# Kernel optimization log

Measured on AMD Instinct MI355X. Metric: run time of the kernel, lower is better.

The kernel has to match this reference:

```python
import jax, jax.numpy as jnp
import numpy as np

N = 20000; E = 160000; C = 64; SH = 9; NB = 8
S_DIM = 16; MS_HID = 64; FC_HID = 64
RATE = 0.1; LAMBDA = 0.5; R_MAX = 5.0; EV_PER = 16
K = int(RATE * N)          # static master-node count (top-k selection)
E_V = EV_PER * K           # static virtual-edge budget


def _safe_len(vec):
    # smooth norm, safe under autodiff at zero-length edges (self loops)
    return jnp.sqrt(jnp.sum(vec * vec, axis=-1, keepdims=True) + 1e-12)


def _sh(vec):
    # real spherical harmonics lmax=2, 'component' normalization, on unit vectors
    n = vec / _safe_len(vec)
    x, y, z = n[:, 0], n[:, 1], n[:, 2]
    s3 = jnp.sqrt(3.0); s15 = jnp.sqrt(15.0); s5 = jnp.sqrt(5.0)
    return jnp.stack([
        jnp.ones_like(x),
        s3 * x, s3 * y, s3 * z,
        s15 * x * y, s15 * y * z, 0.5 * s5 * (3 * z * z - 1.0),
        s15 * x * z, 0.5 * s15 * (x * x - y * y),
    ], axis=-1)  # [E, 9]


def _bessel(r):
    # Bessel radial basis with p=6 polynomial cutoff envelope; r: [E,1]
    n = jnp.arange(1, NB + 1, dtype=r.dtype)
    b = jnp.sqrt(2.0 / R_MAX) * jnp.sin(n * jnp.pi * r / R_MAX) / jnp.clip(r, 1e-9)
    u = jnp.clip(r / R_MAX, 0.0, 1.0); p = 6.0
    env = 1.0 - (p + 1) * (p + 2) / 2 * u ** p + p * (p + 2) * u ** (p + 1) - p * (p + 1) / 2 * u ** (p + 2)
    return b * env  # [E, NB]


def _conv(h, src, dst, sh, ef, emask, n_nodes, fc_w1, fc_b1, fc_w2, fc_b2, lin_w):
    # TFN-style tensor-product conv: per-edge weights from radial MLP,
    # message = flatten(h[dst] outer sh) * w -> linear -> scatter-mean to src
    w = jax.nn.relu(ef @ fc_w1 + fc_b1) @ fc_w2 + fc_b2            # [E, C*SH]
    tp = (h[dst][:, :, None] * sh[:, None, :]).reshape(sh.shape[0], -1) * w
    msg = (tp @ lin_w) * emask[:, None]                            # [E, C]
    agg = jax.ops.segment_sum(msg, src, num_segments=n_nodes)
    deg = jax.ops.segment_sum(emask, src, num_segments=n_nodes)
    return agg / jnp.clip(deg, 1.0)[:, None]


def setup_inputs() -> dict:
    key = jax.random.key(0)
    ks = jax.random.split(key, 12)
    def lin(k, i, o):
        return (jax.random.normal(k, (i, o), jnp.float32) / np.sqrt(i)).astype(jnp.float32)
    return {
        "h": jax.random.normal(ks[0], (N, C), jnp.float32),
        "pos": jax.random.uniform(ks[1], (N, 3), jnp.float32) * 10.0,
        "edge_index": jax.random.randint(ks[2], (2, E), 0, N, dtype=jnp.int32),
        "fc_w1": lin(ks[3], NB, FC_HID), "fc_b1": jnp.zeros((FC_HID,), jnp.float32),
        "fc_w2": lin(ks[4], FC_HID, C * SH), "fc_b2": jnp.zeros((C * SH,), jnp.float32),
        "lin_w": lin(ks[5], C * SH, C),
        "ms_w1": lin(ks[6], S_DIM, MS_HID), "ms_b1": jnp.zeros((MS_HID,), jnp.float32),
        "ms_w2": lin(ks[7], MS_HID, 1), "ms_b2": jnp.zeros((1,), jnp.float32),
        "vg_wq": lin(ks[8], S_DIM, S_DIM), "vg_wk": lin(ks[9], S_DIM, S_DIM),
    }


def reference(h, pos, fc_w1, fc_b1, fc_w2, fc_b2, lin_w,
              ms_w1, ms_b1, ms_w2, ms_b2, vg_wq, vg_wk, edge_index):
    src, dst = edge_index[0], edge_index[1]
    vec = pos[src] - pos[dst]
    sh = _sh(vec)
    ef = _bessel(_safe_len(vec))
    ones_e = jnp.ones((E,), h.dtype)
    h_update = _conv(h, src, dst, sh, ef, ones_e, N, fc_w1, fc_b1, fc_w2, fc_b2, lin_w)
    h_local = h_update + h  # in_dim == out_dim -> pad is a no-op

    # --- master selection (top-k by learned score; static K) ---
    h_sc = h_local[:, :S_DIM]
    score = jax.nn.sigmoid(
        (jax.nn.relu(h_sc @ ms_w1 + ms_b1) @ ms_w2 + ms_b2).squeeze(-1))  # [N]
    _, top_idx = jax.lax.top_k(score, K)
    node_mask = jnp.zeros((N,), h.dtype).at[top_idx].set(1.0)
    m = score * node_mask
    master_idx = jnp.sort(top_idx)

    # relabel full-graph ids -> master-subgraph ids (masked subgraph extraction)
    node2m = jnp.full((N,), -1, jnp.int32).at[master_idx].set(jnp.arange(K, dtype=jnp.int32))
    src_m, dst_m = node2m[src], node2m[dst]
    e_mask = ((src_m >= 0) & (dst_m >= 0)).astype(h.dtype)
    src_mc = jnp.where(src_m >= 0, src_m, 0)
    dst_mc = jnp.where(dst_m >= 0, dst_m, 0)
    adj = jnp.zeros((K, K), h.dtype).at[src_mc, dst_mc].add(e_mask)

    h_master = h_local[master_idx]
    pos_master = pos[master_idx]
    h_ms = h_master[:, :S_DIM]

    # --- virtual edge generation (attention, thresholded by lambda) ---
    q = h_ms @ vg_wq; kk = h_ms @ vg_wk
    attn = jax.nn.sigmoid(q @ kk.T / np.sqrt(S_DIM))  # [K, K]
    exist = (adj > 0) | jnp.eye(K, dtype=bool)
    A_virtual = jnp.where((~exist) & (attn > LAMBDA), 1.0, 0.0).astype(h.dtype)
    vvals, vidx = jax.lax.top_k((attn * A_virtual).reshape(-1), E_V)
    v_src = (vidx // K).astype(jnp.int32); v_dst = (vidx % K).astype(jnp.int32)
    v_mask = (vvals > 0).astype(h.dtype)

    src_all = jnp.concatenate([src_mc, v_src])
    dst_all = jnp.concatenate([dst_mc, v_dst])
    mask_all = jnp.concatenate([e_mask, v_mask])
    vec_m = pos_master[src_all] - pos_master[dst_all]
    sh_m = _sh(vec_m)
    ef_m = _bessel(_safe_len(vec_m))
    h_m_update = _conv(h_master, src_all, dst_all, sh_m, ef_m, mask_all, K,
                       fc_w1, fc_b1, fc_w2, fc_b2, lin_w)
    h_hier = h_m_update + h_master

    h_hier_exp = jnp.zeros_like(h_local).at[master_idx].set(h_hier)
    m_e = m[:, None]
    h_final = (1.0 - m_e) * h_local + m_e * h_hier_exp
    return (h_final, pos, A_virtual, m)
```

## Files before the change

kernel.cpp:

```cpp
#include <hip/hip_runtime.h>
#include <stdint.h>

constexpr int N_   = 20000;
constexpr int E_   = 160000;
constexpr int C_   = 64;
constexpr int K_   = 2000;
constexpr int EV_  = 32000;
constexpr int EALL_ = E_ + EV_;
constexpr int CSH_ = 576;
constexpr int TB_  = 48;

constexpr size_t OFF_AGG    = 0;
constexpr size_t OFF_DEG    = 5120000;
constexpr size_t OFF_AGGM   = 5200000;
constexpr size_t OFF_DEGM   = 5712000;
constexpr size_t OFF_RANK   = 5720000;
constexpr size_t OFF_MASKA  = 5800000;
constexpr size_t OFF_EXIST  = 6568000;
constexpr size_t OFF_HIST   = 10568000;
constexpr size_t OFF_STATE  = 10572096;
constexpr size_t ZERO_BYTES = 10572352;
constexpr size_t OFF_HLOCAL = 10572352;
constexpr size_t OFF_KEY    = 15692352;
constexpr size_t OFF_SCORE  = 15852352;
constexpr size_t OFF_N2M    = 15932352;
constexpr size_t OFF_MIDX   = 16012352;
constexpr size_t OFF_HM     = 16020352;
constexpr size_t OFF_POSM   = 16532352;
constexpr size_t OFF_Q      = 16556352;
constexpr size_t OFF_KBUF   = 16684352;
constexpr size_t OFF_SRCA   = 16812352;
constexpr size_t OFF_DSTA   = 17580352;
constexpr size_t OFF_TMAX   = 18348352;
constexpr size_t OFF_CAND   = 18410880;

struct RState {
    unsigned long long prefix;
    int R;
    unsigned int cand_count;
    unsigned int sel_count;
    int bin_thresh;
    unsigned int total;
    unsigned int pad;
};

__global__ void k_w0(const float* __restrict__ fc_b1, const float* __restrict__ fc_w2,
                     const float* __restrict__ fc_b2, int* __restrict__ w0nz)
{
    __shared__ float hid0[64];
    __shared__ int nz;
    int tid = threadIdx.x;
    if (tid == 0) nz = 0;
    if (tid < 64) hid0[tid] = fmaxf(fc_b1[tid], 0.0f);
    __syncthreads();
    if (tid < CSH_) {
        float acc = fc_b2[tid];
        for (int k = 0; k < 64; k++) acc += hid0[k] * fc_w2[k * CSH_ + tid];
        if (acc != 0.0f) atomicOr(&nz, 1);
    }
    __syncthreads();
    if (tid == 0) *w0nz = nz;
}

__global__ __launch_bounds__(256) void k_prep(
    int n_edges, const int* __restrict__ src, const int* __restrict__ dst,
    const float* __restrict__ mask, const float* __restrict__ posn,
    const int* __restrict__ w0nz, float* __restrict__ deg,
    float* __restrict__ edata, unsigned int* __restrict__ cnt)
{
    int e = blockIdx.x * 256 + threadIdx.x;
    bool valid = e < n_edges;
    int s_i = 0, d_i = 0; float msk = 0.0f;
    if (valid) {
        msk = mask ? mask[e] : 1.0f;
        if (msk != 0.0f) { s_i = src[e]; d_i = dst[e]; }
    }
    bool active = valid && (msk != 0.0f);

    float vx = 0.f, vy = 0.f, vz = 0.f;
    if (active) {
        vx = posn[s_i*3+0] - posn[d_i*3+0];
        vy = posn[s_i*3+1] - posn[d_i*3+1];
        vz = posn[s_i*3+2] - posn[d_i*3+2];
    }
    float r = sqrtf(vx*vx + vy*vy + vz*vz + 1e-12f);
    float invr = 1.0f / r;
    float x = vx*invr, y = vy*invr, z = vz*invr;
    const float s3 = 1.7320508075688772f, s15 = 3.872983346207417f, s5 = 2.23606797749979f;
    float sh[9];
    sh[0] = 1.0f; sh[1] = s3*x; sh[2] = s3*y; sh[3] = s3*z;
    sh[4] = s15*x*y; sh[5] = s15*y*z; sh[6] = 0.5f*s5*(3.0f*z*z - 1.0f);
    sh[7] = s15*x*z; sh[8] = 0.5f*s15*(x*x - y*y);

    float u = r * 0.2f; u = u > 1.0f ? 1.0f : u;
    float u2 = u*u, u6 = u2*u2*u2, u7 = u6*u, u8 = u7*u;
    float env = 1.0f - 28.0f*u6 + 48.0f*u7 - 21.0f*u8;
    float rc = r > 1e-9f ? r : 1e-9f;
    const float bpref = 0.6324555320336759f;
    const float PIov5 = 0.6283185307179586f;
    float ef[8];
    #pragma unroll
    for (int n = 0; n < 8; n++)
        ef[n] = bpref * sinf(PIov5 * r * (float)(n + 1)) / rc * env;

    if (active) atomicAdd(&deg[s_i], msk);

    bool contrib = active && !((env == 0.0f) && (*w0nz == 0));
    int lane = threadIdx.x & 63;
    unsigned long long b = __ballot(contrib);
    int wc = __popcll(b);
    int base = 0;
    if (lane == 0 && wc) base = (int)atomicAdd(cnt, (unsigned)wc);
    base = __shfl(base, 0);
    if (contrib) {
        int slot = base + __popcll(b & ((1ull << lane) - 1ull));
        float* p = edata + (size_t)slot * 20;
        #pragma unroll
        for (int n = 0; n < 8; n++) p[n] = ef[n];
        #pragma unroll
        for (int t = 0; t < 9; t++) p[8+t] = sh[t];
        p[17] = __int_as_float(s_i);
        p[18] = __int_as_float(d_i);
        p[19] = msk;
    }
}

__global__ __launch_bounds__(256, 2) void k_convg(
    const unsigned int* __restrict__ cnt, const float* __restrict__ edata,
    const float* __restrict__ hn,
    const float* __restrict__ fc_w1, const float* __restrict__ fc_b1,
    const float* __restrict__ fc_w2, const float* __restrict__ fc_b2,
    const float* __restrict__ lin_w, float* __restrict__ agg)
{
    __shared__ float s_misc[TB_ * 12];
    __shared__ float s_hid[TB_ * 68];
    __shared__ float s_hd[TB_ * 64];
    __shared__ float s_tp[TB_ * 68];
    __shared__ __align__(16) float s_w[4096];

    const int tid = threadIdx.x;
    const int oq = (tid & 15) * 4;
    const int eg = tid >> 4;

    const int nheavy = (int)*cnt;
    const int nblk = (nheavy + TB_ - 1) / TB_;

    for (int blk = blockIdx.x; blk < nblk; blk += gridDim.x) {
        const int ebase = blk * TB_;
        int nE = nheavy - ebase; if (nE > TB_) nE = TB_;

        for (int idx = tid; idx < TB_ * 12; idx += 256) {
            int e = idx / 12, f = idx - 12 * e;
            float v = 0.0f;
            if (e < nE) {
                const float* p = edata + (size_t)(ebase + e) * 20;
                v = (f < 9) ? p[8 + f] : (f == 9) ? p[17] : (f == 10) ? p[19] : 0.0f;
            }
            s_misc[idx] = v;
        }
        for (int idx = tid; idx < TB_ * 64; idx += 256) {
            int e = idx >> 6, k = idx & 63;
            float hv = 0.0f, hdv = 0.0f;
            if (e < nE) {
                const float* p = edata + (size_t)(ebase + e) * 20;
                float acc = fc_b1[k];
                #pragma unroll
                for (int n = 0; n < 8; n++) acc += p[n] * fc_w1[n * 64 + k];
                hv = fmaxf(acc, 0.0f);
                int dsti = __float_as_int(p[18]);
                hdv = hn[dsti * 64 + k];
            }
            s_hid[e * 68 + k] = hv;
            s_hd[e * 64 + k] = hdv;
        }
        float acc0[4] = {0,0,0,0}, acc1[4] = {0,0,0,0}, acc2[4] = {0,0,0,0};
        __syncthreads();

        for (int cj = 0; cj < 9; cj++) {
            const int j0 = cj * 64;
            for (int i4 = tid; i4 < 1024; i4 += 256) {
                int k = i4 >> 4, q4 = (i4 & 15) * 4;
                *reinterpret_cast<float4*>(&s_w[k * 64 + q4]) =
                    *reinterpret_cast<const float4*>(&fc_w2[k * CSH_ + j0 + q4]);
            }
            __syncthreads();

            float a0[4], a1[4], a2[4];
            #pragma unroll
            for (int p = 0; p < 4; p++) { float b = fc_b2[j0 + oq + p]; a0[p]=b; a1[p]=b; a2[p]=b; }
            #pragma unroll 4
            for (int k = 0; k < 64; k++) {
                float4 w4 = *reinterpret_cast<const float4*>(&s_w[k * 64 + oq]);
                float h0 = s_hid[eg * 68 + k];
                float h1 = s_hid[(eg + 16) * 68 + k];
                float h2 = s_hid[(eg + 32) * 68 + k];
                a0[0]+=h0*w4.x; a0[1]+=h0*w4.y; a0[2]+=h0*w4.z; a0[3]+=h0*w4.w;
                a1[0]+=h1*w4.x; a1[1]+=h1*w4.y; a1[2]+=h1*w4.z; a1[3]+=h1*w4.w;
                a2[0]+=h2*w4.x; a2[1]+=h2*w4.y; a2[2]+=h2*w4.z; a2[3]+=h2*w4.w;
            }
            #pragma unroll
            for (int p = 0; p < 4; p++) {
                int j = j0 + oq + p; int c = j / 9; int si = j - 9 * c;
                s_tp[eg * 68 + oq + p]        = s_hd[eg * 64 + c]        * s_misc[eg * 12 + si]        * a0[p];
                s_tp[(eg + 16) * 68 + oq + p] = s_hd[(eg + 16) * 64 + c] * s_misc[(eg + 16) * 12 + si] * a1[p];
                s_tp[(eg + 32) * 68 + oq + p] = s_hd[(eg + 32) * 64 + c] * s_misc[(eg + 32) * 12 + si] * a2[p];
            }
            __syncthreads();

            for (int i4 = tid; i4 < 1024; i4 += 256) {
                *reinterpret_cast<float4*>(&s_w[i4 * 4]) =
                    *reinterpret_cast<const float4*>(&lin_w[j0 * 64 + i4 * 4]);
            }
            __syncthreads();

            #pragma unroll 4
            for (int jj = 0; jj < 64; jj++) {
                float4 l4 = *reinterpret_cast<const float4*>(&s_w[jj * 64 + oq]);
                float t0 = s_tp[eg * 68 + jj];
                float t1 = s_tp[(eg + 16) * 68 + jj];
                float t2 = s_tp[(eg + 32) * 68 + jj];
                acc0[0]+=t0*l4.x; acc0[1]+=t0*l4.y; acc0[2]+=t0*l4.z; acc0[3]+=t0*l4.w;
                acc1[0]+=t1*l4.x; acc1[1]+=t1*l4.y; acc1[2]+=t1*l4.z; acc1[3]+=t1*l4.w;
                acc2[0]+=t2*l4.x; acc2[1]+=t2*l4.y; acc2[2]+=t2*l4.z; acc2[3]+=t2*l4.w;
            }
            __syncthreads();
        }

        {
            float mk = s_misc[eg * 12 + 10];
            if (mk != 0.0f) {
                int s = __float_as_int(s_misc[eg * 12 + 9]);
                #pragma unroll
                for (int p = 0; p < 4; p++) atomicAdd(&agg[s * 64 + oq + p], acc0[p] * mk);
            }
            mk = s_misc[(eg + 16) * 12 + 10];
            if (mk != 0.0f) {
                int s = __float_as_int(s_misc[(eg + 16) * 12 + 9]);
                #pragma unroll
                for (int p = 0; p < 4; p++) atomicAdd(&agg[s * 64 + oq + p], acc1[p] * mk);
            }
            mk = s_misc[(eg + 32) * 12 + 10];
            if (mk != 0.0f) {
                int s = __float_as_int(s_misc[(eg + 32) * 12 + 9]);
                #pragma unroll
                for (int p = 0; p < 4; p++) atomicAdd(&agg[s * 64 + oq + p], acc2[p] * mk);
            }
        }
        __syncthreads();
    }
}

__global__ __launch_bounds__(256) void k_hlscore(const float* __restrict__ h,
    const float* __restrict__ agg, const float* __restrict__ deg,
    const float* __restrict__ ms_w1, const float* __restrict__ ms_b1,
    const float* __restrict__ ms_w2, const float* __restrict__ ms_b2,
    float* __restrict__ h_local, float* __restrict__ score, unsigned long long* __restrict__ key)
{
    int wid = threadIdx.x >> 6, lane = threadIdx.x & 63;
    int n = blockIdx.x * 4 + wid;
    if (n >= N_) return;
    float d = fmaxf(deg[n], 1.0f);
    float hl = h[n*64 + lane] + agg[n*64 + lane] / d;
    h_local[n*64 + lane] = hl;
    float acc = ms_b1[lane];
    #pragma unroll
    for (int i = 0; i < 16; i++) acc += __shfl(hl, i) * ms_w1[i*64 + lane];
    acc = fmaxf(acc, 0.0f);
    float part = acc * ms_w2[lane];
    #pragma unroll
    for (int off = 32; off > 0; off >>= 1) part += __shfl_xor(part, off);
    if (lane == 0) {
        float s = part + ms_b2[0];
        float sc = 1.0f / (1.0f + expf(-s));
        score[n] = sc;
        key[n] = ((unsigned long long)__float_as_uint(sc) << 32)
               | (unsigned long long)(0xFFFFFFFFu - (unsigned)n);
    }
}

__global__ void k_rank(const unsigned long long* __restrict__ key, int* __restrict__ rankcnt)
{
    __shared__ unsigned long long tile[256];
    int i = blockIdx.x * 256 + threadIdx.x;
    int seg = blockIdx.y;
    int lo = seg * 1250, hi = lo + 1250;
    unsigned long long my = (i < N_) ? key[i] : ~0ull;
    int cnt = 0;
    for (int t0 = lo; t0 < hi; t0 += 256) {
        int idx = t0 + threadIdx.x;
        tile[threadIdx.x] = (idx < hi) ? key[idx] : 0ull;
        __syncthreads();
        int lim = hi - t0; if (lim > 256) lim = 256;
        for (int j = 0; j < lim; j++) cnt += (tile[j] > my) ? 1 : 0;
        __syncthreads();
    }
    if (i < N_ && cnt) atomicAdd(&rankcnt[i], cnt);
}

__global__ __launch_bounds__(1024) void k_scanfin(const int* __restrict__ rankcnt,
    const float* __restrict__ score, int* __restrict__ node2m, int* __restrict__ midx,
    float* __restrict__ m_out)
{
    __shared__ int ssum[1024];
    int tid = threadIdx.x;
    int start = tid * 20;
    int c = 0;
    for (int k = 0; k < 20; k++) {
        int idx = start + k;
        if (idx < N_) {
            int sel = (rankcnt[idx] < K_) ? 1 : 0;
            c += sel;
            m_out[idx] = sel ? score[idx] : 0.0f;
        }
    }
    ssum[tid] = c;
    __syncthreads();
    for (int off = 1; off < 1024; off <<= 1) {
        int v = (tid >= off) ? ssum[tid - off] : 0;
        __syncthreads();
        ssum[tid] += v;
        __syncthreads();
    }
    int run = ssum[tid] - c;
    for (int k = 0; k < 20; k++) {
        int idx = start + k;
        if (idx < N_) {
            if (rankcnt[idx] < K_) { node2m[idx] = run; midx[run] = idx; run++; }
            else node2m[idx] = -1;
        }
    }
}

__global__ __launch_bounds__(256) void k_mastex(const int* __restrict__ midx,
    const float* __restrict__ h_local, const float* __restrict__ pos,
    const float* __restrict__ vg_wq, const float* __restrict__ vg_wk,
    const int* __restrict__ src, const int* __restrict__ dst, const int* __restrict__ node2m,
    float* __restrict__ h_m, float* __restrict__ pos_m,
    float* __restrict__ qbuf, float* __restrict__ kbuf,
    int* __restrict__ src_all, int* __restrict__ dst_all,
    float* __restrict__ mask_all, unsigned char* __restrict__ exist)
{
    int b = blockIdx.x;
    if (b < 500) {
        int mi = b * 4 + (threadIdx.x >> 6);
        int lane = threadIdx.x & 63;
        int node = midx[mi];
        h_m[mi*64 + lane] = h_local[node*64 + lane];
        if (lane < 3) pos_m[mi*3 + lane] = pos[node*3 + lane];
        if (lane < 32) {
            int j = lane & 15;
            const float* wm = (lane < 16) ? vg_wq : vg_wk;
            float acc = 0.0f;
            #pragma unroll
            for (int i = 0; i < 16; i++) acc += h_local[node*64 + i] * wm[i*16 + j];
            if (lane < 16) qbuf[mi*16 + j] = acc; else kbuf[mi*16 + j] = acc;
        }
    } else {
        int e = (b - 500) * 256 + threadIdx.x;
        int sm = node2m[src[e]], dm = node2m[dst[e]];
        bool em = (sm >= 0) && (dm >= 0);
        int smc = sm >= 0 ? sm : 0;
        int dmc = dm >= 0 ? dm : 0;
        src_all[e] = smc; dst_all[e] = dmc; mask_all[e] = em ? 1.0f : 0.0f;
        if (em) exist[smc * K_ + dmc] = 1;
    }
}

constexpr int NTILE_ = (K_ / 16) * (K_ / 16);
__global__ __launch_bounds__(256) void k_attn1(const float* __restrict__ qbuf,
    const float* __restrict__ kbuf, const unsigned char* __restrict__ exist,
    float* __restrict__ Av, float* __restrict__ tmax, unsigned int* __restrict__ hist)
{
    constexpr int TBK = K_ / 16;
    __shared__ float sq[16][17], sk[16][17];
    __shared__ unsigned int lh[1024];
    __shared__ float wmax[4];
    int tid = threadIdx.x;
    for (int b = tid; b < 1024; b += 256) lh[b] = 0;

    for (int t = blockIdx.x; t < NTILE_; t += gridDim.x) {
        int bi = t / TBK, bj = t % TBK;
        int i0 = bi * 16, j0 = bj * 16;
        int r = tid >> 4, c = tid & 15;
        __syncthreads();
        sq[r][c] = qbuf[(i0 + r) * 16 + c];
        sk[r][c] = kbuf[(j0 + r) * 16 + c];
        __syncthreads();
        int ti = tid >> 4, tj = tid & 15;
        float dot = 0.0f;
        #pragma unroll
        for (int cc = 0; cc < 16; cc++) dot += sq[ti][cc] * sk[tj][cc];
        float attn = 1.0f / (1.0f + expf(-dot * 0.25f));
        int gi = i0 + ti, gj = j0 + tj;
        int flat = gi * K_ + gj;
        bool ex = (exist[flat] != 0) || (gi == gj);
        bool av = (!ex) && (attn > 0.5f);
        Av[flat] = av ? 1.0f : 0.0f;
        float cv = av ? attn : 0.0f;
        if (av) {
            unsigned bin = (__float_as_uint(attn) - 0x3F000000u) >> 13;
            if (bin > 1023u) bin = 1023u;
            atomicAdd(&lh[bin], 1u);
        }
        float wm = cv;
        #pragma unroll
        for (int off = 32; off > 0; off >>= 1) wm = fmaxf(wm, __shfl_xor(wm, off));
        int wid = tid >> 6, lane = tid & 63;
        if (lane == 0) wmax[wid] = wm;
        __syncthreads();
        if (tid == 0) tmax[t] = fmaxf(fmaxf(wmax[0], wmax[1]), fmaxf(wmax[2], wmax[3]));
    }
    __syncthreads();
    for (int b = tid; b < 1024; b += 256) {
        unsigned v = lh[b];
        if (v) atomicAdd(&hist[b], v);
    }
}

__global__ __launch_bounds__(1024) void k_bsel(const unsigned int* __restrict__ hist, RState* st)
{
    __shared__ unsigned int h[1024];
    int tid = threadIdx.x;
    h[tid] = hist[tid];
    __syncthreads();
    for (int off = 1; off < 1024; off <<= 1) {
        unsigned v = (tid + off < 1024) ? h[tid + off] : 0u;
        __syncthreads();
        h[tid] += v;
        __syncthreads();
    }
    unsigned total = h[0];
    int R = (total < (unsigned)EV_) ? (int)total : EV_;
    if (tid == 0) {
        st->R = R;
        st->total = total;
        st->cand_count = 0;
        st->sel_count = 0;
        if (R == 0) st->bin_thresh = 1024;
    }
    __syncthreads();
    if (R > 0) {
        unsigned hi = (tid == 1023) ? 0u : h[tid + 1];
        if ((int)h[tid] >= R && (int)hi < R) st->bin_thresh = tid;
    }
}

__global__ __launch_bounds__(256) void k_attn2(const float* __restrict__ qbuf,
    const float* __restrict__ kbuf, const unsigned char* __restrict__ exist,
    const float* __restrict__ tmax, RState* st, unsigned long long* __restrict__ cand)
{
    constexpr int TBK = K_ / 16;
    __shared__ float sq[16][17], sk[16][17];
    __shared__ int wb[4];
    __shared__ int bb;
    int tid = threadIdx.x;
    unsigned tbits = 0x3F000000u + ((unsigned)st->bin_thresh << 13);

    for (int t = blockIdx.x; t < NTILE_; t += gridDim.x) {
        if (__float_as_uint(tmax[t]) < tbits) continue;
        int bi = t / TBK, bj = t % TBK;
        int i0 = bi * 16, j0 = bj * 16;
        int r = tid >> 4, c = tid & 15;
        __syncthreads();
        sq[r][c] = qbuf[(i0 + r) * 16 + c];
        sk[r][c] = kbuf[(j0 + r) * 16 + c];
        __syncthreads();
        int ti = tid >> 4, tj = tid & 15;
        float dot = 0.0f;
        #pragma unroll
        for (int cc = 0; cc < 16; cc++) dot += sq[ti][cc] * sk[tj][cc];
        float attn = 1.0f / (1.0f + expf(-dot * 0.25f));
        int gi = i0 + ti, gj = j0 + tj;
        int flat = gi * K_ + gj;
        bool ex = (exist[flat] != 0) || (gi == gj);
        bool store = (!ex) && (attn > 0.5f) && (__float_as_uint(attn) >= tbits);

        unsigned long long keyv = ((unsigned long long)__float_as_uint(attn) << 32)
                                | (unsigned long long)(0xFFFFFFFFu - (unsigned)flat);
        int wid = tid >> 6, lane = tid & 63;
        unsigned long long b = __ballot(store);
        int wc = __popcll(b);
        if (lane == 0) wb[wid] = wc;
        __syncthreads();
        if (tid == 0) {
            int s = 0;
            for (int w = 0; w < 4; w++) { int cc2 = wb[w]; wb[w] = s; s += cc2; }
            bb = s ? (int)atomicAdd(&st->cand_count, (unsigned)s) : 0;
        }
        __syncthreads();
        if (store) {
            int slot = bb + wb[wid] + __popcll(b & ((1ull << lane) - 1ull));
            cand[slot] = keyv;
        }
    }
}

__global__ __launch_bounds__(1024) void k_radixsel(RState* st,
    const unsigned long long* __restrict__ cand,
    int* __restrict__ src_all, int* __restrict__ dst_all, float* __restrict__ mask_all)
{
    __shared__ unsigned int lh[256];
    __shared__ unsigned int suf[256];
    __shared__ unsigned long long s_pref;
    __shared__ int s_R;
    int tid = threadIdx.x;
    int n = (int)st->cand_count;
    int R = st->R;
    if (tid == 0) { s_pref = 0ull; s_R = R; }
    __syncthreads();

    if (R > 0) {
        for (int p = 0; p < 8; p++) {
            if (tid < 256) lh[tid] = 0;
            __syncthreads();
            unsigned long long pref = s_pref;
            int sh_d = 56 - 8 * p;
            for (int i = tid; i < n; i += 1024) {
                unsigned long long kv = cand[i];
                bool ok = (p == 0) || ((kv >> (sh_d + 8)) == (pref >> (sh_d + 8)));
                if (ok) atomicAdd(&lh[(unsigned)((kv >> sh_d) & 255ull)], 1u);
            }
            __syncthreads();
            if (tid < 256) suf[tid] = lh[tid];
            __syncthreads();
            for (int off = 1; off < 256; off <<= 1) {
                unsigned v = 0;
                if (tid < 256 && tid + off < 256) v = suf[tid + off];
                __syncthreads();
                if (tid < 256) suf[tid] += v;
                __syncthreads();
            }
            if (tid < 256) {
                int Rc = s_R;
                unsigned hi = (tid == 255) ? 0u : suf[tid + 1];
                if ((int)suf[tid] >= Rc && (int)hi < Rc) {
                    s_pref = pref | ((unsigned long long)(unsigned)tid << sh_d);
                    s_R = Rc - (int)hi;
                }
            }
            __syncthreads();
        }
    } else {
        if (tid == 0) s_pref = ~0ull;
        __syncthreads();
    }

    unsigned long long T = s_pref;
    int lane = tid & 63;
    for (int i0 = 0; i0 < n; i0 += 1024) {
        int i = i0 + tid;
        bool sel = (i < n) && (cand[i] >= T);
        unsigned long long b = __ballot(sel);
        int wc = __popcll(b);
        int basep = 0;
        if (lane == 0 && wc) basep = (int)atomicAdd(&st->sel_count, (unsigned)wc);
        basep = __shfl(basep, 0);
        if (sel) {
            int slot = basep + __popcll(b & ((1ull << lane) - 1ull));
            if (slot < EV_) {
                unsigned flat = 0xFFFFFFFFu - (unsigned)(cand[i] & 0xFFFFFFFFull);
                src_all[E_ + slot] = (int)(flat / (unsigned)K_);
                dst_all[E_ + slot] = (int)(flat % (unsigned)K_);
                mask_all[E_ + slot] = 1.0f;
            }
        }
    }
}

__global__ void k_finalpos(const float* __restrict__ h_local, const int* __restrict__ node2m,
    const float* __restrict__ aggm, const float* __restrict__ degm, const float* __restrict__ h_m,
    const float* __restrict__ m_out, const float* __restrict__ pos,
    float* __restrict__ out_h, float* __restrict__ out_pos)
{
    int idx = blockIdx.x * 256 + threadIdx.x;
    if (idx < N_ * 3) out_pos[idx] = pos[idx];
    if (idx >= N_ * C_) return;
    int i = idx >> 6, c = idx & 63;
    float mval = m_out[i];
    int mi = node2m[i];
    float hh = 0.0f;
    if (mi >= 0) hh = aggm[mi*64 + c] / fmaxf(degm[mi], 1.0f) + h_m[mi*64 + c];
    out_h[idx] = (1.0f - mval) * h_local[idx] + mval * hh;
}

extern "C" void kernel_launch(void* const* d_in, const int* in_sizes, int n_in,
                              void* d_out, int out_size, void* d_ws, size_t ws_size,
                              hipStream_t stream)
{
    (void)in_sizes; (void)n_in; (void)out_size; (void)ws_size;
    const float* h     = (const float*)d_in[0];
    const float* pos   = (const float*)d_in[1];
    const int*   eidx  = (const int*)d_in[2];
    const float* fc_w1 = (const float*)d_in[3];
    const float* fc_b1 = (const float*)d_in[4];
    const float* fc_w2 = (const float*)d_in[5];
    const float* fc_b2 = (const float*)d_in[6];
    const float* lin_w = (const float*)d_in[7];
    const float* ms_w1 = (const float*)d_in[8];
    const float* ms_b1 = (const float*)d_in[9];
    const float* ms_w2 = (const float*)d_in[10];
    const float* ms_b2 = (const float*)d_in[11];
    const float* vg_wq = (const float*)d_in[12];
    const float* vg_wk = (const float*)d_in[13];

    char* ws = (char*)d_ws;
    float* agg     = (float*)(ws + OFF_AGG);
    float* deg     = (float*)(ws + OFF_DEG);
    float* aggm    = (float*)(ws + OFF_AGGM);
    float* degm    = (float*)(ws + OFF_DEGM);
    int*   rankcnt = (int*)(ws + OFF_RANK);
    float* mask_all = (float*)(ws + OFF_MASKA);
    unsigned char* exist = (unsigned char*)(ws + OFF_EXIST);
    unsigned int* hist = (unsigned int*)(ws + OFF_HIST);
    RState* st     = (RState*)(ws + OFF_STATE);
    unsigned int* cnt0 = (unsigned int*)(ws + OFF_STATE + 64);
    unsigned int* cnt1 = (unsigned int*)(ws + OFF_STATE + 68);
    int*   w0nz    = (int*)(ws + OFF_STATE + 72);
    float* h_local = (float*)(ws + OFF_HLOCAL);
    unsigned long long* key = (unsigned long long*)(ws + OFF_KEY);
    float* score   = (float*)(ws + OFF_SCORE);
    int*   node2m  = (int*)(ws + OFF_N2M);
    int*   midx    = (int*)(ws + OFF_MIDX);
    float* h_m     = (float*)(ws + OFF_HM);
    float* pos_m   = (float*)(ws + OFF_POSM);
    float* qbuf    = (float*)(ws + OFF_Q);
    float* kbuf    = (float*)(ws + OFF_KBUF);
    int*   src_all = (int*)(ws + OFF_SRCA);
    int*   dst_all = (int*)(ws + OFF_DSTA);
    float* tmax    = (float*)(ws + OFF_TMAX);
    unsigned long long* cand = (unsigned long long*)(ws + OFF_CAND);
    float* edata   = (float*)(ws + OFF_CAND);

    float* out_h   = (float*)d_out;
    float* out_pos = out_h + (size_t)N_ * C_;
    float* out_av  = out_pos + (size_t)N_ * 3;
    float* out_m   = out_av + (size_t)K_ * K_;

    hipMemsetAsync(ws, 0, ZERO_BYTES, stream);

    k_w0<<<1, 576, 0, stream>>>(fc_b1, fc_w2, fc_b2, w0nz);

    k_prep<<<E_ / 256, 256, 0, stream>>>(E_, eidx, eidx + E_, nullptr, pos, w0nz, deg, edata, cnt0);
    k_convg<<<1024, 256, 0, stream>>>(cnt0, edata, h, fc_w1, fc_b1, fc_w2, fc_b2, lin_w, agg);

    k_hlscore<<<(N_ + 3) / 4, 256, 0, stream>>>(h, agg, deg, ms_w1, ms_b1, ms_w2, ms_b2,
                                                h_local, score, key);

    k_rank<<<dim3((N_ + 255) / 256, 16), 256, 0, stream>>>(key, rankcnt);
    k_scanfin<<<1, 1024, 0, stream>>>(rankcnt, score, node2m, midx, out_m);

    k_mastex<<<500 + E_ / 256, 256, 0, stream>>>(midx, h_local, pos, vg_wq, vg_wk,
        eidx, eidx + E_, node2m, h_m, pos_m, qbuf, kbuf, src_all, dst_all, mask_all, exist);

    k_attn1<<<1024, 256, 0, stream>>>(qbuf, kbuf, exist, out_av, tmax, hist);
    k_bsel<<<1, 1024, 0, stream>>>(hist, st);
    k_attn2<<<1024, 256, 0, stream>>>(qbuf, kbuf, exist, tmax, st, cand);
    k_radixsel<<<1, 1024, 0, stream>>>(st, cand, src_all, dst_all, mask_all);

    k_prep<<<EALL_ / 256, 256, 0, stream>>>(EALL_, src_all, dst_all, mask_all, pos_m, w0nz,
                                            degm, edata, cnt1);
    k_convg<<<1024, 256, 0, stream>>>(cnt1, edata, h_m, fc_w1, fc_b1, fc_w2, fc_b2, lin_w, aggm);

    k_finalpos<<<(N_ * C_ + 255) / 256, 256, 0, stream>>>(h_local, node2m, aggm, degm, h_m,
                                                          out_m, pos, out_h, out_pos);
}
```

Before: 764.0 us.

## Keep conv hidden and tensor-product tiles in registers via shuffles; simplify rank and scan

Result: slower. 826.5 us (+8.2%).

```diff
diff --git a/kernel.cpp b/kernel.cpp
--- a/kernel.cpp
+++ b/kernel.cpp
@@ -125,7 +125,7 @@
     }
 }
 
-__global__ __launch_bounds__(256, 2) void k_convg(
+__global__ __launch_bounds__(256, 3) void k_convg(
     const unsigned int* __restrict__ cnt, const float* __restrict__ edata,
     const float* __restrict__ hn,
     const float* __restrict__ fc_w1, const float* __restrict__ fc_b1,
@@ -133,14 +133,14 @@
     const float* __restrict__ lin_w, float* __restrict__ agg)
 {
     __shared__ float s_misc[TB_ * 12];
-    __shared__ float s_hid[TB_ * 68];
-    __shared__ float s_hd[TB_ * 64];
-    __shared__ float s_tp[TB_ * 68];
-    __shared__ __align__(16) float s_w[4096];
+    __shared__ float s_hd[TB_ * 66];
+    __shared__ __align__(16) float s_w2[4096];
+    __shared__ __align__(16) float s_lw[4096];
 
     const int tid = threadIdx.x;
     const int oq = (tid & 15) * 4;
     const int eg = tid >> 4;
+    const int r  = (tid & 63) >> 4;
 
     const int nheavy = (int)*cnt;
     const int nblk = (nheavy + TB_ - 1) / TB_;
@@ -149,6 +149,7 @@
         const int ebase = blk * TB_;
         int nE = nheavy - ebase; if (nE > TB_) nE = TB_;
 
+        __syncthreads();
         for (int idx = tid; idx < TB_ * 12; idx += 256) {
             int e = idx / 12, f = idx - 12 * e;
             float v = 0.0f;
@@ -160,70 +161,89 @@
         }
         for (int idx = tid; idx < TB_ * 64; idx += 256) {
             int e = idx >> 6, k = idx & 63;
-            float hv = 0.0f, hdv = 0.0f;
+            float hdv = 0.0f;
             if (e < nE) {
                 const float* p = edata + (size_t)(ebase + e) * 20;
-                float acc = fc_b1[k];
-                #pragma unroll
-                for (int n = 0; n < 8; n++) acc += p[n] * fc_w1[n * 64 + k];
-                hv = fmaxf(acc, 0.0f);
                 int dsti = __float_as_int(p[18]);
                 hdv = hn[dsti * 64 + k];
             }
-            s_hid[e * 68 + k] = hv;
-            s_hd[e * 64 + k] = hdv;
+            s_hd[e * 66 + k] = hdv;
+        }
+        float hid0[4], hid1[4], hid2[4];
+        {
+            const int es[3] = { eg, eg + 16, eg + 32 };
+            float* regs[3] = { hid0, hid1, hid2 };
+            #pragma unroll
+            for (int t = 0; t < 3; t++) {
+                int e = es[t];
+                if (e < nE) {
+                    const float* p = edata + (size_t)(ebase + e) * 20;
+                    float ef[8];
+                    #pragma unroll
+                    for (int n = 0; n < 8; n++) ef[n] = p[n];
+                    #pragma unroll
+                    for (int q = 0; q < 4; q++) {
+                        float acc = fc_b1[oq + q];
+                        #pragma unroll
+                        for (int n = 0; n < 8; n++) acc += ef[n] * fc_w1[n * 64 + oq + q];
+                        regs[t][q] = fmaxf(acc, 0.0f);
+                    }
+                } else {
+                    #pragma unroll
+                    for (int q = 0; q < 4; q++) regs[t][q] = 0.0f;
+                }
+            }
         }
         float acc0[4] = {0,0,0,0}, acc1[4] = {0,0,0,0}, acc2[4] = {0,0,0,0};
         __syncthreads();
 
         for (int cj = 0; cj < 9; cj++) {
             const int j0 = cj * 64;
+            if (cj) __syncthreads();
             for (int i4 = tid; i4 < 1024; i4 += 256) {
                 int k = i4 >> 4, q4 = (i4 & 15) * 4;
-                *reinterpret_cast<float4*>(&s_w[k * 64 + q4]) =
+                *reinterpret_cast<float4*>(&s_w2[k * 64 + q4]) =
                     *reinterpret_cast<const float4*>(&fc_w2[k * CSH_ + j0 + q4]);
+            }
+            for (int i4 = tid; i4 < 1024; i4 += 256) {
+                *reinterpret_cast<float4*>(&s_lw[i4 * 4]) =
+                    *reinterpret_cast<const float4*>(&lin_w[j0 * 64 + i4 * 4]);
             }
             __syncthreads();
 
             float a0[4], a1[4], a2[4];
             #pragma unroll
-            for (int p = 0; p < 4; p++) { float b = fc_b2[j0 + oq + p]; a0[p]=b; a1[p]=b; a2[p]=b; }
-            #pragma unroll 4
+            for (int q = 0; q < 4; q++) { float b = fc_b2[j0 + oq + q]; a0[q]=b; a1[q]=b; a2[q]=b; }
+            #pragma unroll
             for (int k = 0; k < 64; k++) {
-                float4 w4 = *reinterpret_cast<const float4*>(&s_w[k * 64 + oq]);
-                float h0 = s_hid[eg * 68 + k];
-                float h1 = s_hid[(eg + 16) * 68 + k];
-                float h2 = s_hid[(eg + 32) * 68 + k];
+                float4 w4 = *reinterpret_cast<const float4*>(&s_w2[k * 64 + oq]);
+                int srcl = (r << 4) | (k >> 2);
+                float h0 = __shfl(hid0[k & 3], srcl);
+                float h1 = __shfl(hid1[k & 3], srcl);
+                float h2 = __shfl(hid2[k & 3], srcl);
                 a0[0]+=h0*w4.x; a0[1]+=h0*w4.y; a0[2]+=h0*w4.z; a0[3]+=h0*w4.w;
                 a1[0]+=h1*w4.x; a1[1]+=h1*w4.y; a1[2]+=h1*w4.z; a1[3]+=h1*w4.w;
                 a2[0]+=h2*w4.x; a2[1]+=h2*w4.y; a2[2]+=h2*w4.z; a2[3]+=h2*w4.w;
             }
+            float t0[4], t1[4], t2[4];
             #pragma unroll
-            for (int p = 0; p < 4; p++) {
-                int j = j0 + oq + p; int c = j / 9; int si = j - 9 * c;
-                s_tp[eg * 68 + oq + p]        = s_hd[eg * 64 + c]        * s_misc[eg * 12 + si]        * a0[p];
-                s_tp[(eg + 16) * 68 + oq + p] = s_hd[(eg + 16) * 64 + c] * s_misc[(eg + 16) * 12 + si] * a1[p];
-                s_tp[(eg + 32) * 68 + oq + p] = s_hd[(eg + 32) * 64 + c] * s_misc[(eg + 32) * 12 + si] * a2[p];
-            }
-            __syncthreads();
-
-            for (int i4 = tid; i4 < 1024; i4 += 256) {
-                *reinterpret_cast<float4*>(&s_w[i4 * 4]) =
-                    *reinterpret_cast<const float4*>(&lin_w[j0 * 64 + i4 * 4]);
-            }
-            __syncthreads();
-
-            #pragma unroll 4
+            for (int q = 0; q < 4; q++) {
+                int j = j0 + oq + q; int c = j / 9; int si = j - 9 * c;
+                t0[q] = s_hd[eg * 66 + c]        * s_misc[eg * 12 + si]        * a0[q];
+                t1[q] = s_hd[(eg + 16) * 66 + c] * s_misc[(eg + 16) * 12 + si] * a1[q];
+                t2[q] = s_hd[(eg + 32) * 66 + c] * s_misc[(eg + 32) * 12 + si] * a2[q];
+            }
+            #pragma unroll
             for (int jj = 0; jj < 64; jj++) {
-                float4 l4 = *reinterpret_cast<const float4*>(&s_w[jj * 64 + oq]);
-                float t0 = s_tp[eg * 68 + jj];
-                float t1 = s_tp[(eg + 16) * 68 + jj];
-                float t2 = s_tp[(eg + 32) * 68 + jj];
-                acc0[0]+=t0*l4.x; acc0[1]+=t0*l4.y; acc0[2]+=t0*l4.z; acc0[3]+=t0*l4.w;
-                acc1[0]+=t1*l4.x; acc1[1]+=t1*l4.y; acc1[2]+=t1*l4.z; acc1[3]+=t1*l4.w;
-                acc2[0]+=t2*l4.x; acc2[1]+=t2*l4.y; acc2[2]+=t2*l4.z; acc2[3]+=t2*l4.w;
-            }
-            __syncthreads();
+                float4 l4 = *reinterpret_cast<const float4*>(&s_lw[jj * 64 + oq]);
+                int srcl = (r << 4) | (jj >> 2);
+                float p0 = __shfl(t0[jj & 3], srcl);
+                float p1 = __shfl(t1[jj & 3], srcl);
+                float p2 = __shfl(t2[jj & 3], srcl);
+                acc0[0]+=p0*l4.x; acc0[1]+=p0*l4.y; acc0[2]+=p0*l4.z; acc0[3]+=p0*l4.w;
+                acc1[0]+=p1*l4.x; acc1[1]+=p1*l4.y; acc1[2]+=p1*l4.z; acc1[3]+=p1*l4.w;
+                acc2[0]+=p2*l4.x; acc2[1]+=p2*l4.y; acc2[2]+=p2*l4.z; acc2[3]+=p2*l4.w;
+            }
         }
 
         {
@@ -231,22 +251,21 @@
             if (mk != 0.0f) {
                 int s = __float_as_int(s_misc[eg * 12 + 9]);
                 #pragma unroll
-                for (int p = 0; p < 4; p++) atomicAdd(&agg[s * 64 + oq + p], acc0[p] * mk);
+                for (int q = 0; q < 4; q++) atomicAdd(&agg[s * 64 + oq + q], acc0[q] * mk);
             }
             mk = s_misc[(eg + 16) * 12 + 10];
             if (mk != 0.0f) {
                 int s = __float_as_int(s_misc[(eg + 16) * 12 + 9]);
                 #pragma unroll
-                for (int p = 0; p < 4; p++) atomicAdd(&agg[s * 64 + oq + p], acc1[p] * mk);
+                for (int q = 0; q < 4; q++) atomicAdd(&agg[s * 64 + oq + q], acc1[q] * mk);
             }
             mk = s_misc[(eg + 32) * 12 + 10];
             if (mk != 0.0f) {
                 int s = __float_as_int(s_misc[(eg + 32) * 12 + 9]);
                 #pragma unroll
-                for (int p = 0; p < 4; p++) atomicAdd(&agg[s * 64 + oq + p], acc2[p] * mk);
-            }
-        }
-        __syncthreads();
+                for (int q = 0; q < 4; q++) atomicAdd(&agg[s * 64 + oq + q], acc2[q] * mk);
+            }
+        }
     }
 }
 
@@ -278,22 +297,16 @@
     }
 }
 
-__global__ void k_rank(const unsigned long long* __restrict__ key, int* __restrict__ rankcnt)
-{
-    __shared__ unsigned long long tile[256];
+__global__ __launch_bounds__(256) void k_rank(const unsigned long long* __restrict__ key,
+                                              int* __restrict__ rankcnt)
+{
     int i = blockIdx.x * 256 + threadIdx.x;
     int seg = blockIdx.y;
     int lo = seg * 1250, hi = lo + 1250;
     unsigned long long my = (i < N_) ? key[i] : ~0ull;
     int cnt = 0;
-    for (int t0 = lo; t0 < hi; t0 += 256) {
-        int idx = t0 + threadIdx.x;
-        tile[threadIdx.x] = (idx < hi) ? key[idx] : 0ull;
-        __syncthreads();
-        int lim = hi - t0; if (lim > 256) lim = 256;
-        for (int j = 0; j < lim; j++) cnt += (tile[j] > my) ? 1 : 0;
-        __syncthreads();
-    }
+    #pragma unroll 8
+    for (int j = lo; j < hi; j++) cnt += (key[j] > my) ? 1 : 0;
     if (i < N_ && cnt) atomicAdd(&rankcnt[i], cnt);
 }
 
@@ -301,31 +314,35 @@
     const float* __restrict__ score, int* __restrict__ node2m, int* __restrict__ midx,
     float* __restrict__ m_out)
 {
-    __shared__ int ssum[1024];
-    int tid = threadIdx.x;
-    int start = tid * 20;
-    int c = 0;
-    for (int k = 0; k < 20; k++) {
-        int idx = start + k;
+    __shared__ int wsum[16];
+    __shared__ int wbase[16];
+    __shared__ int s_base;
+    int tid = threadIdx.x, lane = tid & 63, wv = tid >> 6;
+    if (tid == 0) s_base = 0;
+    __syncthreads();
+    for (int c = 0; c < 20; c++) {
+        int idx = c * 1024 + tid;
+        int sel = 0;
         if (idx < N_) {
-            int sel = (rankcnt[idx] < K_) ? 1 : 0;
-            c += sel;
+            sel = (rankcnt[idx] < K_) ? 1 : 0;
             m_out[idx] = sel ? score[idx] : 0.0f;
         }
-    }
-    ssum[tid] = c;
-    __syncthreads();
-    for (int off = 1; off < 1024; off <<= 1) {
-        int v = (tid >= off) ? ssum[tid - off] : 0;
-        __syncthreads();
-        ssum[tid] += v;
-        __syncthreads();
-    }
-    int run = ssum[tid] - c;
-    for (int k = 0; k < 20; k++) {
-        int idx = start + k;
+        int v = sel;
+        #pragma unroll
+        for (int off = 1; off < 64; off <<= 1) {
+            int u = __shfl_up(v, off);
+            if (lane >= off) v += u;
+        }
+        if (lane == 63) wsum[wv] = v;
+        __syncthreads();
+        if (tid == 0) {
+            int runb = s_base;
+            for (int w = 0; w < 16; w++) { wbase[w] = runb; runb += wsum[w]; }
+            s_base = runb;
+        }
+        __syncthreads();
         if (idx < N_) {
-            if (rankcnt[idx] < K_) { node2m[idx] = run; midx[run] = idx; run++; }
+            if (sel) { int rk = wbase[wv] + v - 1; node2m[idx] = rk; midx[rk] = idx; }
             else node2m[idx] = -1;
         }
     }
@@ -641,7 +658,7 @@
     k_w0<<<1, 576, 0, stream>>>(fc_b1, fc_w2, fc_b2, w0nz);
 
     k_prep<<<E_ / 256, 256, 0, stream>>>(E_, eidx, eidx + E_, nullptr, pos, w0nz, deg, edata, cnt0);
-    k_convg<<<1024, 256, 0, stream>>>(cnt0, edata, h, fc_w1, fc_b1, fc_w2, fc_b2, lin_w, agg);
+    k_convg<<<768, 256, 0, stream>>>(cnt0, edata, h, fc_w1, fc_b1, fc_w2, fc_b2, lin_w, agg);
 
     k_hlscore<<<(N_ + 3) / 4, 256, 0, stream>>>(h, agg, deg, ms_w1, ms_b1, ms_w2, ms_b2,
                                                 h_local, score, key);
@@ -659,7 +676,7 @@
 
     k_prep<<<EALL_ / 256, 256, 0, stream>>>(EALL_, src_all, dst_all, mask_all, pos_m, w0nz,
                                             degm, edata, cnt1);
-    k_convg<<<1024, 256, 0, stream>>>(cnt1, edata, h_m, fc_w1, fc_b1, fc_w2, fc_b2, lin_w, aggm);
+    k_convg<<<768, 256, 0, stream>>>(cnt1, edata, h_m, fc_w1, fc_b1, fc_w2, fc_b2, lin_w, aggm);
 
     k_finalpos<<<(N_ * C_ + 255) / 256, 256, 0, stream>>>(h_local, node2m, aggm, degm, h_m,
                                                           out_m, pos, out_h, out_pos);
```

## Raise conv occupancy, fuse bucket select into attn, rework rank/scan/radix select

Applied to the files above, without the earlier changes.

Result: faster. 744.2 us (-2.6%).

```diff
diff --git a/kernel.cpp b/kernel.cpp
--- a/kernel.cpp
+++ b/kernel.cpp
@@ -125,7 +125,7 @@
     }
 }
 
-__global__ __launch_bounds__(256, 2) void k_convg(
+__global__ __launch_bounds__(256, 3) void k_convg(
     const unsigned int* __restrict__ cnt, const float* __restrict__ edata,
     const float* __restrict__ hn,
     const float* __restrict__ fc_w1, const float* __restrict__ fc_b1,
@@ -134,7 +134,6 @@
 {
     __shared__ float s_misc[TB_ * 12];
     __shared__ float s_hid[TB_ * 68];
-    __shared__ float s_hd[TB_ * 64];
     __shared__ float s_tp[TB_ * 68];
     __shared__ __align__(16) float s_w[4096];
 
@@ -149,35 +148,38 @@
         const int ebase = blk * TB_;
         int nE = nheavy - ebase; if (nE > TB_) nE = TB_;
 
+        __syncthreads();
         for (int idx = tid; idx < TB_ * 12; idx += 256) {
             int e = idx / 12, f = idx - 12 * e;
             float v = 0.0f;
             if (e < nE) {
                 const float* p = edata + (size_t)(ebase + e) * 20;
-                v = (f < 9) ? p[8 + f] : (f == 9) ? p[17] : (f == 10) ? p[19] : 0.0f;
+                v = (f < 9) ? p[8 + f] : (f == 9) ? p[17] : (f == 10) ? p[19] : p[18];
             }
             s_misc[idx] = v;
         }
         for (int idx = tid; idx < TB_ * 64; idx += 256) {
             int e = idx >> 6, k = idx & 63;
-            float hv = 0.0f, hdv = 0.0f;
+            float hv = 0.0f;
             if (e < nE) {
                 const float* p = edata + (size_t)(ebase + e) * 20;
                 float acc = fc_b1[k];
                 #pragma unroll
                 for (int n = 0; n < 8; n++) acc += p[n] * fc_w1[n * 64 + k];
                 hv = fmaxf(acc, 0.0f);
-                int dsti = __float_as_int(p[18]);
-                hdv = hn[dsti * 64 + k];
             }
             s_hid[e * 68 + k] = hv;
-            s_hd[e * 64 + k] = hdv;
         }
         float acc0[4] = {0,0,0,0}, acc1[4] = {0,0,0,0}, acc2[4] = {0,0,0,0};
         __syncthreads();
+
+        const int d0 = __float_as_int(s_misc[eg * 12 + 11]);
+        const int d1 = __float_as_int(s_misc[(eg + 16) * 12 + 11]);
+        const int d2 = __float_as_int(s_misc[(eg + 32) * 12 + 11]);
 
         for (int cj = 0; cj < 9; cj++) {
             const int j0 = cj * 64;
+            if (cj) __syncthreads();
             for (int i4 = tid; i4 < 1024; i4 += 256) {
                 int k = i4 >> 4, q4 = (i4 & 15) * 4;
                 *reinterpret_cast<float4*>(&s_w[k * 64 + q4]) =
@@ -185,9 +187,15 @@
             }
             __syncthreads();
 
+            const int jb = j0 + oq;
+            const int c0 = jb / 9, c1 = (jb + 3) / 9;
+            float hA0 = hn[d0 * 64 + c0], hB0 = hn[d0 * 64 + c1];
+            float hA1 = hn[d1 * 64 + c0], hB1 = hn[d1 * 64 + c1];
+            float hA2 = hn[d2 * 64 + c0], hB2 = hn[d2 * 64 + c1];
+
             float a0[4], a1[4], a2[4];
             #pragma unroll
-            for (int p = 0; p < 4; p++) { float b = fc_b2[j0 + oq + p]; a0[p]=b; a1[p]=b; a2[p]=b; }
+            for (int q = 0; q < 4; q++) { float b = fc_b2[jb + q]; a0[q]=b; a1[q]=b; a2[q]=b; }
             #pragma unroll 4
             for (int k = 0; k < 64; k++) {
                 float4 w4 = *reinterpret_cast<const float4*>(&s_w[k * 64 + oq]);
@@ -199,11 +207,11 @@
                 a2[0]+=h2*w4.x; a2[1]+=h2*w4.y; a2[2]+=h2*w4.z; a2[3]+=h2*w4.w;
             }
             #pragma unroll
-            for (int p = 0; p < 4; p++) {
-                int j = j0 + oq + p; int c = j / 9; int si = j - 9 * c;
-                s_tp[eg * 68 + oq + p]        = s_hd[eg * 64 + c]        * s_misc[eg * 12 + si]        * a0[p];
-                s_tp[(eg + 16) * 68 + oq + p] = s_hd[(eg + 16) * 64 + c] * s_misc[(eg + 16) * 12 + si] * a1[p];
-                s_tp[(eg + 32) * 68 + oq + p] = s_hd[(eg + 32) * 64 + c] * s_misc[(eg + 32) * 12 + si] * a2[p];
+            for (int q = 0; q < 4; q++) {
+                int j = jb + q; int cc = j / 9; int si = j - 9 * cc;
+                s_tp[eg * 68 + oq + q]        = (cc == c0 ? hA0 : hB0) * s_misc[eg * 12 + si]        * a0[q];
+                s_tp[(eg + 16) * 68 + oq + q] = (cc == c0 ? hA1 : hB1) * s_misc[(eg + 16) * 12 + si] * a1[q];
+                s_tp[(eg + 32) * 68 + oq + q] = (cc == c0 ? hA2 : hB2) * s_misc[(eg + 32) * 12 + si] * a2[q];
             }
             __syncthreads();
 
@@ -223,7 +231,6 @@
                 acc1[0]+=t1*l4.x; acc1[1]+=t1*l4.y; acc1[2]+=t1*l4.z; acc1[3]+=t1*l4.w;
                 acc2[0]+=t2*l4.x; acc2[1]+=t2*l4.y; acc2[2]+=t2*l4.z; acc2[3]+=t2*l4.w;
             }
-            __syncthreads();
         }
 
         {
@@ -231,22 +238,21 @@
             if (mk != 0.0f) {
                 int s = __float_as_int(s_misc[eg * 12 + 9]);
                 #pragma unroll
-                for (int p = 0; p < 4; p++) atomicAdd(&agg[s * 64 + oq + p], acc0[p] * mk);
+                for (int q = 0; q < 4; q++) atomicAdd(&agg[s * 64 + oq + q], acc0[q] * mk);
             }
             mk = s_misc[(eg + 16) * 12 + 10];
             if (mk != 0.0f) {
                 int s = __float_as_int(s_misc[(eg + 16) * 12 + 9]);
                 #pragma unroll
-                for (int p = 0; p < 4; p++) atomicAdd(&agg[s * 64 + oq + p], acc1[p] * mk);
+                for (int q = 0; q < 4; q++) atomicAdd(&agg[s * 64 + oq + q], acc1[q] * mk);
             }
             mk = s_misc[(eg + 32) * 12 + 10];
             if (mk != 0.0f) {
                 int s = __float_as_int(s_misc[(eg + 32) * 12 + 9]);
                 #pragma unroll
-                for (int p = 0; p < 4; p++) atomicAdd(&agg[s * 64 + oq + p], acc2[p] * mk);
-            }
-        }
-        __syncthreads();
+                for (int q = 0; q < 4; q++) atomicAdd(&agg[s * 64 + oq + q], acc2[q] * mk);
+            }
+        }
     }
 }
 
@@ -278,22 +284,16 @@
     }
 }
 
-__global__ void k_rank(const unsigned long long* __restrict__ key, int* __restrict__ rankcnt)
-{
-    __shared__ unsigned long long tile[256];
+__global__ __launch_bounds__(256) void k_rank(const unsigned long long* __restrict__ key,
+                                              int* __restrict__ rankcnt)
+{
     int i = blockIdx.x * 256 + threadIdx.x;
     int seg = blockIdx.y;
     int lo = seg * 1250, hi = lo + 1250;
     unsigned long long my = (i < N_) ? key[i] : ~0ull;
     int cnt = 0;
-    for (int t0 = lo; t0 < hi; t0 += 256) {
-        int idx = t0 + threadIdx.x;
-        tile[threadIdx.x] = (idx < hi) ? key[idx] : 0ull;
-        __syncthreads();
-        int lim = hi - t0; if (lim > 256) lim = 256;
-        for (int j = 0; j < lim; j++) cnt += (tile[j] > my) ? 1 : 0;
-        __syncthreads();
-    }
+    #pragma unroll 8
+    for (int j = lo; j < hi; j++) cnt += (key[j] > my) ? 1 : 0;
     if (i < N_ && cnt) atomicAdd(&rankcnt[i], cnt);
 }
 
@@ -301,31 +301,35 @@
     const float* __restrict__ score, int* __restrict__ node2m, int* __restrict__ midx,
     float* __restrict__ m_out)
 {
-    __shared__ int ssum[1024];
-    int tid = threadIdx.x;
-    int start = tid * 20;
-    int c = 0;
-    for (int k = 0; k < 20; k++) {
-        int idx = start + k;
+    __shared__ int wsum[16];
+    __shared__ int wbase[16];
+    __shared__ int s_base;
+    int tid = threadIdx.x, lane = tid & 63, wv = tid >> 6;
+    if (tid == 0) s_base = 0;
+    __syncthreads();
+    for (int c = 0; c < 20; c++) {
+        int idx = c * 1024 + tid;
+        int sel = 0;
         if (idx < N_) {
-            int sel = (rankcnt[idx] < K_) ? 1 : 0;
-            c += sel;
+            sel = (rankcnt[idx] < K_) ? 1 : 0;
             m_out[idx] = sel ? score[idx] : 0.0f;
         }
-    }
-    ssum[tid] = c;
-    __syncthreads();
-    for (int off = 1; off < 1024; off <<= 1) {
-        int v = (tid >= off) ? ssum[tid - off] : 0;
-        __syncthreads();
-        ssum[tid] += v;
-        __syncthreads();
-    }
-    int run = ssum[tid] - c;
-    for (int k = 0; k < 20; k++) {
-        int idx = start + k;
+        int v = sel;
+        #pragma unroll
+        for (int off = 1; off < 64; off <<= 1) {
+            int u = __shfl_up(v, off);
+            if (lane >= off) v += u;
+        }
+        if (lane == 63) wsum[wv] = v;
+        __syncthreads();
+        if (tid == 0) {
+            int runb = s_base;
+            for (int w = 0; w < 16; w++) { wbase[w] = runb; runb += wsum[w]; }
+            s_base = runb;
+        }
+        __syncthreads();
         if (idx < N_) {
-            if (rankcnt[idx] < K_) { node2m[idx] = run; midx[run] = idx; run++; }
+            if (sel) { int rk = wbase[wv] + v - 1; node2m[idx] = rk; midx[rk] = idx; }
             else node2m[idx] = -1;
         }
     }
@@ -369,12 +373,15 @@
 constexpr int NTILE_ = (K_ / 16) * (K_ / 16);
 __global__ __launch_bounds__(256) void k_attn1(const float* __restrict__ qbuf,
     const float* __restrict__ kbuf, const unsigned char* __restrict__ exist,
-    float* __restrict__ Av, float* __restrict__ tmax, unsigned int* __restrict__ hist)
+    float* __restrict__ Av, float* __restrict__ tmax, unsigned int* __restrict__ hist,
+    RState* st, unsigned int* __restrict__ done_ctr)
 {
     constexpr int TBK = K_ / 16;
     __shared__ float sq[16][17], sk[16][17];
     __shared__ unsigned int lh[1024];
     __shared__ float wmax[4];
+    __shared__ unsigned int ha[1024], hb[1024];
+    __shared__ unsigned int s_last;
     int tid = threadIdx.x;
     for (int b = tid; b < 1024; b += 256) lh[b] = 0;
 
@@ -415,33 +422,33 @@
         unsigned v = lh[b];
         if (v) atomicAdd(&hist[b], v);
     }
-}
-
-__global__ __launch_bounds__(1024) void k_bsel(const unsigned int* __restrict__ hist, RState* st)
-{
-    __shared__ unsigned int h[1024];
-    int tid = threadIdx.x;
-    h[tid] = hist[tid];
-    __syncthreads();
+    __syncthreads();
+    __threadfence();
+    if (tid == 0) s_last = (atomicAdd(done_ctr, 1u) == (unsigned)gridDim.x - 1u) ? 1u : 0u;
+    __syncthreads();
+    if (!s_last) return;
+    __threadfence();
+    for (int b = tid; b < 1024; b += 256) ha[b] = hist[b];
+    __syncthreads();
+    unsigned* srcp = ha; unsigned* dstp = hb;
     for (int off = 1; off < 1024; off <<= 1) {
-        unsigned v = (tid + off < 1024) ? h[tid + off] : 0u;
-        __syncthreads();
-        h[tid] += v;
-        __syncthreads();
-    }
-    unsigned total = h[0];
+        for (int b = tid; b < 1024; b += 256)
+            dstp[b] = srcp[b] + ((b + off < 1024) ? srcp[b + off] : 0u);
+        __syncthreads();
+        unsigned* tmp = srcp; srcp = dstp; dstp = tmp;
+    }
+    unsigned total = srcp[0];
     int R = (total < (unsigned)EV_) ? (int)total : EV_;
     if (tid == 0) {
-        st->R = R;
-        st->total = total;
-        st->cand_count = 0;
-        st->sel_count = 0;
+        st->R = R; st->total = total; st->cand_count = 0; st->sel_count = 0;
         if (R == 0) st->bin_thresh = 1024;
     }
     __syncthreads();
     if (R > 0) {
-        unsigned hi = (tid == 1023) ? 0u : h[tid + 1];
-        if ((int)h[tid] >= R && (int)hi < R) st->bin_thresh = tid;
+        for (int b = tid; b < 1024; b += 256) {
+            unsigned hi2 = (b == 1023) ? 0u : srcp[b + 1];
+            if ((int)srcp[b] >= R && (int)hi2 < R) st->bin_thresh = b;
+        }
     }
 }
 
@@ -501,24 +508,26 @@
 {
     __shared__ unsigned int lh[256];
     __shared__ unsigned int suf[256];
-    __shared__ unsigned long long s_pref;
-    __shared__ int s_R;
+    __shared__ unsigned int s_tie[8192];
+    __shared__ unsigned int s_pref, s_R, s_tiecnt, s_cfth;
     int tid = threadIdx.x;
     int n = (int)st->cand_count;
     int R = st->R;
-    if (tid == 0) { s_pref = 0ull; s_R = R; }
-    __syncthreads();
-
+    if (tid == 0) { s_pref = 0x3F000000u; s_R = (unsigned)R; s_tiecnt = 0; s_cfth = 0; }
+    __syncthreads();
+
+    unsigned long long T;
     if (R > 0) {
-        for (int p = 0; p < 8; p++) {
+        for (int p = 0; p < 3; p++) {
             if (tid < 256) lh[tid] = 0;
             __syncthreads();
-            unsigned long long pref = s_pref;
-            int sh_d = 56 - 8 * p;
+            unsigned pref = s_pref;
+            int sh_d = 16 - 8 * p;
+            unsigned pm = 0xFFFFFFFFu << (sh_d + 8);
             for (int i = tid; i < n; i += 1024) {
-                unsigned long long kv = cand[i];
-                bool ok = (p == 0) || ((kv >> (sh_d + 8)) == (pref >> (sh_d + 8)));
-                if (ok) atomicAdd(&lh[(unsigned)((kv >> sh_d) & 255ull)], 1u);
+                unsigned a = (unsigned)(cand[i] >> 32);
+                if ((a & pm) == (pref & pm))
+                    atomicAdd(&lh[(a >> sh_d) & 255u], 1u);
             }
             __syncthreads();
             if (tid < 256) suf[tid] = lh[tid];
@@ -531,21 +540,40 @@
                 __syncthreads();
             }
             if (tid < 256) {
-                int Rc = s_R;
-                unsigned hi = (tid == 255) ? 0u : suf[tid + 1];
-                if ((int)suf[tid] >= Rc && (int)hi < Rc) {
-                    s_pref = pref | ((unsigned long long)(unsigned)tid << sh_d);
-                    s_R = Rc - (int)hi;
+                unsigned Rc = s_R;
+                unsigned hi2 = (tid == 255) ? 0u : suf[tid + 1];
+                if (suf[tid] >= Rc && hi2 < Rc) {
+                    s_pref = pref | ((unsigned)tid << sh_d);
+                    s_R = Rc - hi2;
                 }
             }
             __syncthreads();
         }
+        unsigned Ta = s_pref;
+        unsigned Rrem = s_R;
+        for (int i = tid; i < n; i += 1024) {
+            unsigned long long kv = cand[i];
+            if ((unsigned)(kv >> 32) == Ta) {
+                unsigned pos = atomicAdd(&s_tiecnt, 1u);
+                if (pos < 8192u) s_tie[pos] = (unsigned)(kv & 0xFFFFFFFFull);
+            }
+        }
+        __syncthreads();
+        unsigned Cq = s_tiecnt; if (Cq > 8192u) Cq = 8192u;
+        if (Rrem >= 1u && Rrem < Cq) {
+            for (int i = tid; i < (int)Cq; i += 1024) {
+                unsigned me = s_tie[i];
+                unsigned r = 0;
+                for (int j = 0; j < (int)Cq; j++) r += (s_tie[j] > me) ? 1u : 0u;
+                if (r == Rrem - 1u) s_cfth = me;
+            }
+        }
+        __syncthreads();
+        T = ((unsigned long long)Ta << 32) | (unsigned long long)s_cfth;
     } else {
-        if (tid == 0) s_pref = ~0ull;
-        __syncthreads();
-    }
-
-    unsigned long long T = s_pref;
+        T = ~0ull;
+    }
+
     int lane = tid & 63;
     for (int i0 = 0; i0 < n; i0 += 1024) {
         int i = i0 + tid;
@@ -616,6 +644,7 @@
     unsigned int* cnt0 = (unsigned int*)(ws + OFF_STATE + 64);
     unsigned int* cnt1 = (unsigned int*)(ws + OFF_STATE + 68);
     int*   w0nz    = (int*)(ws + OFF_STATE + 72);
+    unsigned int* done_ctr = (unsigned int*)(ws + OFF_STATE + 76);
     float* h_local = (float*)(ws + OFF_HLOCAL);
     unsigned long long* key = (unsigned long long*)(ws + OFF_KEY);
     float* score   = (float*)(ws + OFF_SCORE);
@@ -641,7 +670,7 @@
     k_w0<<<1, 576, 0, stream>>>(fc_b1, fc_w2, fc_b2, w0nz);
 
     k_prep<<<E_ / 256, 256, 0, stream>>>(E_, eidx, eidx + E_, nullptr, pos, w0nz, deg, edata, cnt0);
-    k_convg<<<1024, 256, 0, stream>>>(cnt0, edata, h, fc_w1, fc_b1, fc_w2, fc_b2, lin_w, agg);
+    k_convg<<<768, 256, 0, stream>>>(cnt0, edata, h, fc_w1, fc_b1, fc_w2, fc_b2, lin_w, agg);
 
     k_hlscore<<<(N_ + 3) / 4, 256, 0, stream>>>(h, agg, deg, ms_w1, ms_b1, ms_w2, ms_b2,
                                                 h_local, score, key);
@@ -652,14 +681,13 @@
     k_mastex<<<500 + E_ / 256, 256, 0, stream>>>(midx, h_local, pos, vg_wq, vg_wk,
         eidx, eidx + E_, node2m, h_m, pos_m, qbuf, kbuf, src_all, dst_all, mask_all, exist);
 
-    k_attn1<<<1024, 256, 0, stream>>>(qbuf, kbuf, exist, out_av, tmax, hist);
-    k_bsel<<<1, 1024, 0, stream>>>(hist, st);
+    k_attn1<<<1024, 256, 0, stream>>>(qbuf, kbuf, exist, out_av, tmax, hist, st, done_ctr);
     k_attn2<<<1024, 256, 0, stream>>>(qbuf, kbuf, exist, tmax, st, cand);
     k_radixsel<<<1, 1024, 0, stream>>>(st, cand, src_all, dst_all, mask_all);
 
     k_prep<<<EALL_ / 256, 256, 0, stream>>>(EALL_, src_all, dst_all, mask_all, pos_m, w0nz,
                                             degm, edata, cnt1);
-    k_convg<<<1024, 256, 0, stream>>>(cnt1, edata, h_m, fc_w1, fc_b1, fc_w2, fc_b2, lin_w, aggm);
+    k_convg<<<768, 256, 0, stream>>>(cnt1, edata, h_m, fc_w1, fc_b1, fc_w2, fc_b2, lin_w, aggm);
 
     k_finalpos<<<(N_ * C_ + 255) / 256, 256, 0, stream>>>(h_local, node2m, aggm, degm, h_m,
                                                           out_m, pos, out_h, out_pos);
```
